# Performance work log

Measured on AMD Instinct MI355X. Metric: run time of the kernel, lower is better.

Reference implementation:

```python
import jax, jax.numpy as jnp
import numpy as np

N, E, DIN, H, DOUT = 100000, 400000, 128, 128, 128
LN_EPS = 1e-5


def _layernorm(x, g, b):
    m = jnp.mean(x, axis=-1, keepdims=True)
    v = jnp.mean((x - m) ** 2, axis=-1, keepdims=True)
    return (x - m) * jax.lax.rsqrt(v + LN_EPS) * g + b


def setup_inputs() -> dict:
    key = jax.random.key(0)
    ks = jax.random.split(key, 24)
    s = 1.0 / np.sqrt(H)
    inp = {
        'feat': jax.random.normal(ks[0], (N, DIN), jnp.float32),
        'edge_src': jax.random.randint(ks[1], (E,), 0, N, jnp.int32),
        'edge_dst': jax.random.randint(ks[2], (E,), 0, N, jnp.int32),
        'W_src': jax.random.normal(ks[3], (DIN, H), jnp.float32) * s,
        'b_src': jax.random.normal(ks[4], (H,), jnp.float32) * s,
        'W_dst': jax.random.normal(ks[5], (DIN, H), jnp.float32) * s,
        'b_dst': jax.random.normal(ks[6], (H,), jnp.float32) * s,
        'W1a': jax.random.normal(ks[7], (H, H), jnp.float32) * s,
        'W1b': jax.random.normal(ks[8], (H, H), jnp.float32) * s,
        'b1': jax.random.normal(ks[9], (H,), jnp.float32) * s,
        'W2': jax.random.normal(ks[10], (H, H), jnp.float32) * s,
        'b2': jax.random.normal(ks[11], (H,), jnp.float32) * s,
        'W3': jax.random.normal(ks[12], (H, H), jnp.float32) * s,
        'b3': jax.random.normal(ks[13], (H,), jnp.float32) * s,
        'ln_g': jnp.ones((H,), jnp.float32),
        'ln_b': jnp.zeros((H,), jnp.float32),
        'Wg1a': jax.random.normal(ks[14], (H, H), jnp.float32) * s,
        'Wg1b': jax.random.normal(ks[15], (H, H), jnp.float32) * s,
        'bg1': jax.random.normal(ks[16], (H,), jnp.float32) * s,
        'Wg2': jax.random.normal(ks[17], (H, 1), jnp.float32) * s,
        'bg2': jax.random.normal(ks[18], (1,), jnp.float32) * s,
        'W_out': jax.random.normal(ks[19], (H, DOUT), jnp.float32) * s,
        'b_out': jax.random.normal(ks[20], (DOUT,), jnp.float32) * s,
    }
    return inp


def reference(feat, edge_src, edge_dst, W_src, b_src, W_dst, b_dst,
              W1a, W1b, b1, W2, b2, W3, b3, ln_g, ln_b,
              Wg1a, Wg1b, bg1, Wg2, bg2, W_out, b_out):
    gelu = lambda x: jax.nn.gelu(x, approximate=False)  # torch nn.GELU default (erf)
    # node-level src/dst transforms, then gather per edge
    src_h = feat @ W_src + b_src                 # [N,H]
    dst_h = feat @ W_dst + b_dst                 # [N,H]
    se = src_h[edge_src]                         # [E,H]
    de = dst_h[edge_dst]                         # [E,H]
    # edge MLP on concat([se,de]) expressed as split weights (same math)
    h = gelu(se @ W1a + de @ W1b + b1)           # [E,H]
    h = gelu(h @ W2 + b2)                        # [E,H]
    msg = _layernorm(h @ W3 + b3, ln_g, ln_b)    # [E,H]
    # message gating
    gate = jax.nn.sigmoid(gelu(se @ Wg1a + de @ Wg1b + bg1) @ Wg2 + bg2)  # [E,1]
    msg = gate * msg
    # scatter-sum to destination nodes, then out transform
    upd = jax.ops.segment_sum(msg, edge_dst, num_segments=N)  # [N,H]
    return upd @ W_out + b_out                   # [N,DOUT]
```

## Files before the change

### kernel.cpp

```cpp
#include <hip/hip_runtime.h>
#include <hip/hip_bf16.h>
#include <math.h>


typedef __bf16 bf16x8 __attribute__((ext_vector_type(8)));
typedef __bf16 bf16x2 __attribute__((ext_vector_type(2)));
typedef float floatx4 __attribute__((ext_vector_type(4)));

#define LN_EPS 1e-5f

__device__ __forceinline__ unsigned short f2bf(float x) {
  unsigned int u = __float_as_uint(x);
  u = u + 0x7fffu + ((u >> 16) & 1u);
  return (unsigned short)(u >> 16);
}

__device__ __forceinline__ unsigned int pkbf(float lo, float hi) {
  bf16x2 v;
  v.x = (__bf16)lo;
  v.y = (__bf16)hi;
  return __builtin_bit_cast(unsigned int, v);
}

__device__ __forceinline__ float bf2f(unsigned short s) {
  return __uint_as_float(((unsigned int)s) << 16);
}

__device__ __forceinline__ float geluf(float x) {
  float t = x * x;
  float u = x * (2.3022080f + 0.1029434f * t);
  float e = __builtin_amdgcn_exp2f(-u);
  return x * __builtin_amdgcn_rcpf(1.0f + e);
}

__device__ __forceinline__ float sigmoidf_fast(float x) {
  float e = __builtin_amdgcn_exp2f(-1.44269504f * x);
  return __builtin_amdgcn_rcpf(1.0f + e);
}

__global__ __launch_bounds__(256) void prep_weights(
    const float* w0, const float* w1, const float* w2, const float* w3,
    const float* w4, const float* w5, const float* w6, const float* w7,
    const float* w8, unsigned short* out) {
  const float* srcs[9] = {w0, w1, w2, w3, w4, w5, w6, w7, w8};
  int m = blockIdx.x >> 2, c = blockIdx.x & 3;
  const float* src = srcs[m] + c * 32 * 128;
  __shared__ unsigned short sT[128][35];
  int tid = threadIdx.x;

  for (int it = 0; it < 4; ++it) {
    int f4 = tid + it * 256;
    float4 v = ((const float4*)src)[f4];
    int krel = f4 >> 5;
    int n0 = (f4 & 31) * 4;
    sT[n0 + 0][krel] = f2bf(v.x);
    sT[n0 + 1][krel] = f2bf(v.y);
    sT[n0 + 2][krel] = f2bf(v.z);
    sT[n0 + 3][krel] = f2bf(v.w);
  }
  __syncthreads();
  unsigned short* dst = out + m * 16384 + c * 32;
  for (int it = 0; it < 2; ++it) {
    int ch = tid + it * 256;
    int n = ch >> 2, kc = (ch & 3) * 8;
    unsigned short tmp[8];
    for (int j = 0; j < 8; ++j) tmp[j] = sT[n][kc + j];
    *(int4*)(dst + n * 128 + kc) = *(const int4*)tmp;
  }
}

#define LDB(pB, B)                                              \
  do {                                                          \
    const unsigned short* _p = (pB);                            \
    for (int kb = 0; kb < 4; ++kb) {                            \
      B[0][kb] = *(const bf16x8*)(_p + kb * 32);                \
      B[1][kb] = *(const bf16x8*)(_p + 2048 + kb * 32);         \
    }                                                           \
  } while (0)

__global__ __launch_bounds__(256, 4) void node_fused(
    const float* __restrict__ feat, const unsigned short* __restrict__ wT,
    const float* __restrict__ b_src, const float* __restrict__ b_dst,
    const float* __restrict__ b1, const float* __restrict__ bg1,
    unsigned short* __restrict__ SrcCat, unsigned short* __restrict__ DstCat,
    unsigned short* __restrict__ upd, int M) {
  __shared__ __align__(16) unsigned short sF[64][136];
  __shared__ __align__(16) unsigned short sT[64][136];
  int tid = threadIdx.x;
  int r0 = blockIdx.x * 64;

  {
    int4 z = {0, 0, 0, 0};
    int4* p = (int4*)(upd + (long long)r0 * 128);
    for (int it = 0; it < 4; ++it) {
      int idx = tid + it * 256;
      if (r0 + (idx >> 4) < M) p[idx] = z;
    }
  }

  {
    int r = tid >> 2, seg = tid & 3;
    int row = r0 + r;
    const float* src = feat + (long long)row * 128 + seg * 32;
    for (int j = 0; j < 4; ++j) {
      unsigned int tmp[4];
      if (row < M) {
        float4 f0 = *(const float4*)(src + j * 8);
        float4 f1 = *(const float4*)(src + j * 8 + 4);
        tmp[0] = pkbf(f0.x, f0.y);
        tmp[1] = pkbf(f0.z, f0.w);
        tmp[2] = pkbf(f1.x, f1.y);
        tmp[3] = pkbf(f1.z, f1.w);
      } else {
        tmp[0] = tmp[1] = tmp[2] = tmp[3] = 0;
      }
      *(int4*)&sF[r][seg * 32 + j * 8] = *(const int4*)tmp;
    }
  }
  __syncthreads();

  int w = tid >> 6, lane = tid & 63, lr = lane & 15, q = lane >> 4;
  int c0 = 32 * w + lr, c1 = c0 + 16;
  const unsigned short* pB = wT + c0 * 128 + q * 8;

  bf16x8 B[2][4];
  floatx4 accA[4][2], accP[4][2];

  auto zac = [&](floatx4 (&acc)[4][2]) {
    for (int mb = 0; mb < 4; ++mb)
      for (int nb = 0; nb < 2; ++nb) acc[mb][nb] = (floatx4){0.f, 0.f, 0.f, 0.f};
  };
  auto pass = [&](const unsigned short (*Ab)[136], floatx4 (&acc)[4][2]) {
    for (int kb = 0; kb < 4; ++kb) {
      int k = kb * 32 + q * 8;
      for (int mb = 0; mb < 4; ++mb) {
        bf16x8 a = *(const bf16x8*)&Ab[16 * mb + lr][k];
        acc[mb][0] = __builtin_amdgcn_mfma_f32_16x16x32_bf16(a, B[0][kb], acc[mb][0], 0, 0, 0);
        acc[mb][1] = __builtin_amdgcn_mfma_f32_16x16x32_bf16(a, B[1][kb], acc[mb][1], 0, 0, 0);
      }
    }
  };
  auto stage_out = [&](unsigned short (*S)[136], floatx4 (&acc)[4][2],
                       float bb0, float bb1) {
    for (int mb = 0; mb < 4; ++mb)
      for (int i = 0; i < 4; ++i) {
        int r = 16 * mb + 4 * q + i;
        unsigned int u = pkbf(acc[mb][0][i] + bb0, acc[mb][1][i] + bb1);
        S[r][c0] = (unsigned short)u;
        S[r][c1] = (unsigned short)(u >> 16);
      }
  };
  auto copy_half = [&](unsigned short* dstbase,
                       const unsigned short (*S)[136]) {
    for (int it = 0; it < 4; ++it) {
      int idx = tid + it * 256;
      int row = idx >> 4, c = idx & 15;
      if (r0 + row < M)
        *(int4*)(dstbase + (long long)(r0 + row) * 256 + c * 8) =
            *(const int4*)&S[row][c * 8];
    }
  };

  LDB(pB + 0 * 16384, B);
  zac(accA);
  pass(sF, accA);
  stage_out(sT, accA, b_src[c0], b_src[c1]);
  __syncthreads();

  LDB(pB + 2 * 16384, B);
  zac(accA);
  pass(sT, accA);
  LDB(pB + 6 * 16384, B);
  zac(accP);
  pass(sT, accP);
  __syncthreads();

  stage_out(sT, accA, b1[c0], b1[c1]);
  __syncthreads();
  copy_half(SrcCat, sT);
  __syncthreads();
  stage_out(sT, accP, bg1[c0], bg1[c1]);
  __syncthreads();
  copy_half(SrcCat + 128, sT);
  __syncthreads();

  LDB(pB + 1 * 16384, B);
  zac(accA);
  pass(sF, accA);
  stage_out(sT, accA, b_dst[c0], b_dst[c1]);
  __syncthreads();

  LDB(pB + 3 * 16384, B);
  zac(accA);
  pass(sT, accA);
  LDB(pB + 7 * 16384, B);
  zac(accP);
  pass(sT, accP);
  __syncthreads();

  stage_out(sF, accA, 0.f, 0.f);
  stage_out(sT, accP, 0.f, 0.f);
  __syncthreads();

  copy_half(DstCat, sF);
  copy_half(DstCat + 128, sT);
}

__global__ __launch_bounds__(256, 4) void gemm_out(
    const unsigned short* __restrict__ A, const unsigned short* __restrict__ Bt,
    const float* __restrict__ bias, float* __restrict__ C, int M) {
  __shared__ __align__(16) char smem[64 * 130 * 4];
  unsigned short (*sA)[136] = (unsigned short(*)[136])smem;
  float (*sO)[130] = (float(*)[130])smem;
  int tid = threadIdx.x;
  int r0 = blockIdx.x * 64;

  {
    int r = tid >> 2, seg = tid & 3;
    int row = r0 + r;
    const int4* src = (const int4*)(A + (long long)row * 128);
    for (int it = 0; it < 4; ++it) {
      int c = seg * 4 + it;
      int4 v;
      if (row < M) v = src[c];
      else v = (int4){0, 0, 0, 0};
      *(int4*)&sA[r][c * 8] = v;
    }
  }
  __syncthreads();

  int w = tid >> 6, lane = tid & 63, lr = lane & 15, q = lane >> 4;
  int c0 = 32 * w + lr, c1 = 32 * w + 16 + lr;
  const unsigned short* pB = Bt + c0 * 128 + q * 8;

  bf16x8 B[2][4];
  LDB(pB, B);
  floatx4 acc[4][2];
  for (int mb = 0; mb < 4; ++mb)
    for (int nb = 0; nb < 2; ++nb) acc[mb][nb] = (floatx4){0.f, 0.f, 0.f, 0.f};
  for (int kb = 0; kb < 4; ++kb) {
    int k = kb * 32 + q * 8;
    for (int mb = 0; mb < 4; ++mb) {
      bf16x8 a = *(const bf16x8*)&sA[16 * mb + lr][k];
      acc[mb][0] = __builtin_amdgcn_mfma_f32_16x16x32_bf16(a, B[0][kb], acc[mb][0], 0, 0, 0);
      acc[mb][1] = __builtin_amdgcn_mfma_f32_16x16x32_bf16(a, B[1][kb], acc[mb][1], 0, 0, 0);
    }
  }
  __syncthreads();

  float bv0 = bias[c0], bv1 = bias[c1];
  for (int mb = 0; mb < 4; ++mb)
    for (int i = 0; i < 4; ++i) {
      int r = 16 * mb + 4 * q + i;
      sO[r][c0] = acc[mb][0][i] + bv0;
      sO[r][c1] = acc[mb][1][i] + bv1;
    }
  __syncthreads();

  for (int it = 0; it < 8; ++it) {
    int idx = tid + it * 256;
    int row = idx >> 5, c = idx & 31;
    if (r0 + row < M)
      *(float4*)(C + (long long)(r0 + row) * 128 + c * 4) = *(const float4*)&sO[row][c * 4];
  }
}

__global__ __launch_bounds__(256, 6) void edge_fused(
    const unsigned short* __restrict__ SrcCat, const unsigned short* __restrict__ DstCat,
    const int* __restrict__ edge_src, const int* __restrict__ edge_dst,
    const unsigned short* __restrict__ wT,
    const float* __restrict__ b2, const float* __restrict__ b3,
    const float* __restrict__ ln_g, const float* __restrict__ ln_b,
    const float* __restrict__ Wg2, const float* __restrict__ bg2,
    unsigned short* __restrict__ upd, int E) {
  __shared__ __align__(16) unsigned short sH[64][136];
  __shared__ int sDst[64];
  __shared__ float sGate[64];
  __shared__ float sR1[4][64];
  __shared__ float sR2[4][64];
  __shared__ float sM[64];
  __shared__ float sRS[64];

  int tid = threadIdx.x;
  int e0 = blockIdx.x * 64;

  {
    int r = tid >> 2, seg = tid & 3;
    int e = e0 + r;
    int ee = (e < E) ? e : (E - 1);
    int es = edge_src[ee], ed = edge_dst[ee];
    if (seg == 0) sDst[r] = (e < E) ? ed : -1;
    const unsigned short* ps = SrcCat + (long long)es * 256 + seg * 32;
    const unsigned short* pd = DstCat + (long long)ed * 256 + seg * 32;

    int4 sa[4], sb[4], ga[4], gb[4];
    for (int u = 0; u < 4; ++u) {
      sa[u] = ((const int4*)ps)[u];
      sb[u] = ((const int4*)pd)[u];
      ga[u] = ((const int4*)(ps + 128))[u];
      gb[u] = ((const int4*)(pd + 128))[u];
    }
    for (int u = 0; u < 4; ++u) {
      const unsigned short* av = (const unsigned short*)&sa[u];
      const unsigned short* bv = (const unsigned short*)&sb[u];
      unsigned int ov[4];
      for (int j = 0; j < 4; ++j) {
        float g0 = geluf(bf2f(av[2 * j])     + bf2f(bv[2 * j]));
        float g1 = geluf(bf2f(av[2 * j + 1]) + bf2f(bv[2 * j + 1]));
        ov[j] = pkbf(g0, g1);
      }
      *(int4*)&sH[r][seg * 32 + u * 8] = *(const int4*)ov;
    }
    float gp = 0.f;
    for (int u = 0; u < 4; ++u) {
      const unsigned short* av = (const unsigned short*)&ga[u];
      const unsigned short* bv = (const unsigned short*)&gb[u];
      float4 w0 = *(const float4*)(Wg2 + seg * 32 + u * 8);
      float4 w1 = *(const float4*)(Wg2 + seg * 32 + u * 8 + 4);
      gp += geluf(bf2f(av[0]) + bf2f(bv[0])) * w0.x;
      gp += geluf(bf2f(av[1]) + bf2f(bv[1])) * w0.y;
      gp += geluf(bf2f(av[2]) + bf2f(bv[2])) * w0.z;
      gp += geluf(bf2f(av[3]) + bf2f(bv[3])) * w0.w;
      gp += geluf(bf2f(av[4]) + bf2f(bv[4])) * w1.x;
      gp += geluf(bf2f(av[5]) + bf2f(bv[5])) * w1.y;
      gp += geluf(bf2f(av[6]) + bf2f(bv[6])) * w1.z;
      gp += geluf(bf2f(av[7]) + bf2f(bv[7])) * w1.w;
    }
    gp += __shfl_xor(gp, 1);
    gp += __shfl_xor(gp, 2);
    if (seg == 0) sGate[r] = sigmoidf_fast(gp + bg2[0]);
  }
  __syncthreads();

  int w = tid >> 6, lane = tid & 63, lr = lane & 15, q = lane >> 4;
  int c0 = 32 * w + lr, c1 = 32 * w + 16 + lr;
  const unsigned short* pB = wT + c0 * 128 + q * 8;

  bf16x8 B[2][4];
  floatx4 acc[4][2];
  auto zacc = [&]() {
    for (int mb = 0; mb < 4; ++mb)
      for (int nb = 0; nb < 2; ++nb) acc[mb][nb] = (floatx4){0.f, 0.f, 0.f, 0.f};
  };
  auto pass = [&](const unsigned short (*Ab)[136]) {
    for (int kb = 0; kb < 4; ++kb) {
      int k = kb * 32 + q * 8;
      for (int mb = 0; mb < 4; ++mb) {
        bf16x8 a = *(const bf16x8*)&Ab[16 * mb + lr][k];
        acc[mb][0] = __builtin_amdgcn_mfma_f32_16x16x32_bf16(a, B[0][kb], acc[mb][0], 0, 0, 0);
        acc[mb][1] = __builtin_amdgcn_mfma_f32_16x16x32_bf16(a, B[1][kb], acc[mb][1], 0, 0, 0);
      }
    }
  };

  LDB(pB + 4 * 16384, B);
  zacc();
  pass(sH);
  __syncthreads();
  {
    float bv0 = b2[c0], bv1 = b2[c1];
    for (int mb = 0; mb < 4; ++mb)
      for (int i = 0; i < 4; ++i) {
        int r = 16 * mb + 4 * q + i;
        unsigned int u = pkbf(geluf(acc[mb][0][i] + bv0), geluf(acc[mb][1][i] + bv1));
        sH[r][c0] = (unsigned short)u;
        sH[r][c1] = (unsigned short)(u >> 16);
      }
  }
  __syncthreads();

  LDB(pB + 5 * 16384, B);
  zacc();
  pass(sH);
  {
    float bv0 = b3[c0], bv1 = b3[c1];
    for (int mb = 0; mb < 4; ++mb)
      for (int i = 0; i < 4; ++i) {
        float x0 = acc[mb][0][i] + bv0;
        float x1 = acc[mb][1][i] + bv1;
        acc[mb][0][i] = x0; acc[mb][1][i] = x1;
        float s = x0 + x1, s2 = x0 * x0 + x1 * x1;
        s += __shfl_xor(s, 1); s += __shfl_xor(s, 2);
        s += __shfl_xor(s, 4); s += __shfl_xor(s, 8);
        s2 += __shfl_xor(s2, 1); s2 += __shfl_xor(s2, 2);
        s2 += __shfl_xor(s2, 4); s2 += __shfl_xor(s2, 8);
        if (lr == 0) { sR1[w][16 * mb + 4 * q + i] = s; sR2[w][16 * mb + 4 * q + i] = s2; }
      }
  }
  __syncthreads();
  if (tid < 64) {
    float s = sR1[0][tid] + sR1[1][tid] + sR1[2][tid] + sR1[3][tid];
    float s2 = sR2[0][tid] + sR2[1][tid] + sR2[2][tid] + sR2[3][tid];
    float m = s * (1.f / 128.f);
    float v = s2 * (1.f / 128.f) - m * m;
    sM[tid] = m;
    sRS[tid] = rsqrtf(v + LN_EPS);
  }
  __syncthreads();

  {
    float lg0 = ln_g[c0], lg1 = ln_g[c1];
    float lb0 = ln_b[c0], lb1 = ln_b[c1];
    for (int mb = 0; mb < 4; ++mb)
      for (int i = 0; i < 4; ++i) {
        int r = 16 * mb + 4 * q + i;
        int dst = sDst[r];
        float m = sM[r], rs = sRS[r], gt = sGate[r];
        float v0 = ((acc[mb][0][i] - m) * rs * lg0 + lb0) * gt;
        float v1 = ((acc[mb][1][i] - m) * rs * lg1 + lb1) * gt;
        float o0 = __shfl_xor(v0, 1);
        float o1 = __shfl_xor(v1, 1);
        if (dst >= 0) {
          unsigned int pk;
          int colb;
          if ((lr & 1) == 0) {
            pk = pkbf(v0, o0);
            colb = c0;
          } else {
            pk = pkbf(o1, v1);
            colb = c0 + 15;
          }
          unsigned short* addr = upd + (long long)dst * 128 + colb;
          asm volatile("global_atomic_pk_add_bf16 %0, %1, off"
                       :: "v"(addr), "v"(pk) : "memory");
        }
      }
  }
}

extern "C" void kernel_launch(void* const* d_in, const int* in_sizes, int n_in,
                              void* d_out, int out_size, void* d_ws, size_t ws_size,
                              hipStream_t stream) {
  const float* feat   = (const float*)d_in[0];
  const int* edge_src = (const int*)d_in[1];
  const int* edge_dst = (const int*)d_in[2];
  const float* W_src = (const float*)d_in[3];  const float* b_src = (const float*)d_in[4];
  const float* W_dst = (const float*)d_in[5];  const float* b_dst = (const float*)d_in[6];
  const float* W1a = (const float*)d_in[7];    const float* W1b = (const float*)d_in[8];
  const float* b1  = (const float*)d_in[9];
  const float* W2  = (const float*)d_in[10];   const float* b2  = (const float*)d_in[11];
  const float* W3  = (const float*)d_in[12];   const float* b3  = (const float*)d_in[13];
  const float* ln_g = (const float*)d_in[14];  const float* ln_b = (const float*)d_in[15];
  const float* Wg1a = (const float*)d_in[16];  const float* Wg1b = (const float*)d_in[17];
  const float* bg1  = (const float*)d_in[18];
  const float* Wg2  = (const float*)d_in[19];  const float* bg2 = (const float*)d_in[20];
  const float* W_out = (const float*)d_in[21]; const float* b_out = (const float*)d_in[22];

  int N = in_sizes[0] / 128;
  int E = in_sizes[1];

  char* ws = (char*)d_ws;
  unsigned short* wT = (unsigned short*)ws;
  size_t off = 9 * 16384 * sizeof(unsigned short);
  unsigned short* SrcCat = (unsigned short*)(ws + off);
  off += (size_t)N * 256 * sizeof(unsigned short);
  unsigned short* DstCat = (unsigned short*)(ws + off);
  off += (size_t)N * 256 * sizeof(unsigned short);
  unsigned short* upd = (unsigned short*)(ws + off);

  prep_weights<<<36, 256, 0, stream>>>(W_src, W_dst, W1a, W1b, W2, W3, Wg1a, Wg1b,
                                       W_out, wT);
  int mtiles = (N + 63) / 64;
  node_fused<<<mtiles, 256, 0, stream>>>(feat, wT, b_src, b_dst, b1, bg1,
                                         SrcCat, DstCat, upd, N);
  edge_fused<<<(E + 63) / 64, 256, 0, stream>>>(SrcCat, DstCat, edge_src, edge_dst,
                                                wT, b2, b3, ln_g, ln_b, Wg2, bg2,
                                                upd, E);
  gemm_out<<<mtiles, 256, 0, stream>>>(upd, wT + 8 * 16384, b_out, (float*)d_out, N);
}
```

Baseline: 393.3 us.

## Restructure node_fused so each wave owns 16 rows, removing block barriers

```diff
diff --git a/kernel.cpp b/kernel.cpp
--- a/kernel.cpp
+++ b/kernel.cpp
@@ -6,6 +6,7 @@
 typedef __bf16 bf16x8 __attribute__((ext_vector_type(8)));
 typedef __bf16 bf16x2 __attribute__((ext_vector_type(2)));
 typedef float floatx4 __attribute__((ext_vector_type(4)));
+typedef unsigned int uintx4 __attribute__((ext_vector_type(4)));
 
 #define LN_EPS 1e-5f
 
@@ -20,6 +21,11 @@
   v.x = (__bf16)lo;
   v.y = (__bf16)hi;
   return __builtin_bit_cast(unsigned int, v);
+}
+
+__device__ __forceinline__ unsigned short f2bfh(float x) {
+  __bf16 h = (__bf16)x;
+  return __builtin_bit_cast(unsigned short, h);
 }
 
 __device__ __forceinline__ float bf2f(unsigned short s) {
@@ -84,76 +90,86 @@
     const float* __restrict__ b1, const float* __restrict__ bg1,
     unsigned short* __restrict__ SrcCat, unsigned short* __restrict__ DstCat,
     unsigned short* __restrict__ upd, int M) {
-  __shared__ __align__(16) unsigned short sF[64][136];
-  __shared__ __align__(16) unsigned short sT[64][136];
+  __shared__ __align__(16) unsigned short sW[4][16][136];
+  __shared__ __align__(16) unsigned short sU[4][16][136];
   int tid = threadIdx.x;
-  int r0 = blockIdx.x * 64;
+  int w = tid >> 6, lane = tid & 63, lr = lane & 15, q = lane >> 4;
+  int r0 = blockIdx.x * 64 + w * 16;
+
+  unsigned short (*mW)[136] = sW[w];
+  unsigned short (*mU)[136] = sU[w];
 
   {
     int4 z = {0, 0, 0, 0};
-    int4* p = (int4*)(upd + (long long)r0 * 128);
-    for (int it = 0; it < 4; ++it) {
-      int idx = tid + it * 256;
-      if (r0 + (idx >> 4) < M) p[idx] = z;
-    }
-  }
-
-  {
-    int r = tid >> 2, seg = tid & 3;
-    int row = r0 + r;
-    const float* src = feat + (long long)row * 128 + seg * 32;
+#pragma unroll
     for (int j = 0; j < 4; ++j) {
-      unsigned int tmp[4];
-      if (row < M) {
-        float4 f0 = *(const float4*)(src + j * 8);
-        float4 f1 = *(const float4*)(src + j * 8 + 4);
-        tmp[0] = pkbf(f0.x, f0.y);
-        tmp[1] = pkbf(f0.z, f0.w);
-        tmp[2] = pkbf(f1.x, f1.y);
-        tmp[3] = pkbf(f1.z, f1.w);
-      } else {
-        tmp[0] = tmp[1] = tmp[2] = tmp[3] = 0;
-      }
-      *(int4*)&sF[r][seg * 32 + j * 8] = *(const int4*)tmp;
-    }
-  }
-  __syncthreads();
-
-  int w = tid >> 6, lane = tid & 63, lr = lane & 15, q = lane >> 4;
-  int c0 = 32 * w + lr, c1 = c0 + 16;
-  const unsigned short* pB = wT + c0 * 128 + q * 8;
-
-  bf16x8 B[2][4];
-  floatx4 accA[4][2], accP[4][2];
-
-  auto zac = [&](floatx4 (&acc)[4][2]) {
-    for (int mb = 0; mb < 4; ++mb)
-      for (int nb = 0; nb < 2; ++nb) acc[mb][nb] = (floatx4){0.f, 0.f, 0.f, 0.f};
-  };
-  auto pass = [&](const unsigned short (*Ab)[136], floatx4 (&acc)[4][2]) {
+      int idx = lane + j * 64;
+      int row = idx >> 4, c = idx & 15;
+      if (r0 + row < M)
+        ((int4*)(upd + (long long)(r0 + row) * 128))[c] = z;
+    }
+  }
+
+  bf16x8 fA[4];
+  {
+    int frow = r0 + lr;
+    bool fok = frow < M;
+    const float* fp = feat + (long long)frow * 128 + q * 8;
+#pragma unroll
     for (int kb = 0; kb < 4; ++kb) {
-      int k = kb * 32 + q * 8;
-      for (int mb = 0; mb < 4; ++mb) {
-        bf16x8 a = *(const bf16x8*)&Ab[16 * mb + lr][k];
-        acc[mb][0] = __builtin_amdgcn_mfma_f32_16x16x32_bf16(a, B[0][kb], acc[mb][0], 0, 0, 0);
-        acc[mb][1] = __builtin_amdgcn_mfma_f32_16x16x32_bf16(a, B[1][kb], acc[mb][1], 0, 0, 0);
-      }
-    }
-  };
-  auto stage_out = [&](unsigned short (*S)[136], floatx4 (&acc)[4][2],
-                       float bb0, float bb1) {
-    for (int mb = 0; mb < 4; ++mb)
-      for (int i = 0; i < 4; ++i) {
-        int r = 16 * mb + 4 * q + i;
-        unsigned int u = pkbf(acc[mb][0][i] + bb0, acc[mb][1][i] + bb1);
-        S[r][c0] = (unsigned short)u;
-        S[r][c1] = (unsigned short)(u >> 16);
-      }
-  };
-  auto copy_half = [&](unsigned short* dstbase,
-                       const unsigned short (*S)[136]) {
-    for (int it = 0; it < 4; ++it) {
-      int idx = tid + it * 256;
+      float4 a = {0.f, 0.f, 0.f, 0.f}, b = {0.f, 0.f, 0.f, 0.f};
+      if (fok) {
+        a = *(const float4*)(fp + kb * 32);
+        b = *(const float4*)(fp + kb * 32 + 4);
+      }
+      uintx4 u;
+      u.x = pkbf(a.x, a.y);
+      u.y = pkbf(a.z, a.w);
+      u.z = pkbf(b.x, b.y);
+      u.w = pkbf(b.z, b.w);
+      fA[kb] = __builtin_bit_cast(bf16x8, u);
+    }
+  }
+
+  floatx4 acc[8];
+  bf16x8 hA[4];
+
+  auto zacc = [&]() {
+#pragma unroll
+    for (int nt = 0; nt < 8; ++nt) acc[nt] = (floatx4){0.f, 0.f, 0.f, 0.f};
+  };
+  auto gemm = [&](const unsigned short* wbase, const bf16x8 (&Af)[4]) {
+#pragma unroll
+    for (int nt = 0; nt < 8; ++nt) {
+      const unsigned short* bp = wbase + (nt * 16 + lr) * 128 + q * 8;
+      bf16x8 B0 = *(const bf16x8*)(bp);
+      bf16x8 B1 = *(const bf16x8*)(bp + 32);
+      bf16x8 B2 = *(const bf16x8*)(bp + 64);
+      bf16x8 B3 = *(const bf16x8*)(bp + 96);
+      acc[nt] = __builtin_amdgcn_mfma_f32_16x16x32_bf16(Af[0], B0, acc[nt], 0, 0, 0);
+      acc[nt] = __builtin_amdgcn_mfma_f32_16x16x32_bf16(Af[1], B1, acc[nt], 0, 0, 0);
+      acc[nt] = __builtin_amdgcn_mfma_f32_16x16x32_bf16(Af[2], B2, acc[nt], 0, 0, 0);
+      acc[nt] = __builtin_amdgcn_mfma_f32_16x16x32_bf16(Af[3], B3, acc[nt], 0, 0, 0);
+    }
+  };
+  auto stage = [&](unsigned short (*S)[136], const float* bias) {
+#pragma unroll
+    for (int nt = 0; nt < 8; ++nt) {
+      float bv = bias ? bias[nt * 16 + lr] : 0.f;
+#pragma unroll
+      for (int i = 0; i < 4; ++i)
+        S[4 * q + i][nt * 16 + lr] = f2bfh(acc[nt][i] + bv);
+    }
+  };
+  auto loadA = [&](unsigned short (*S)[136]) {
+#pragma unroll
+    for (int kb = 0; kb < 4; ++kb)
+      hA[kb] = *(const bf16x8*)&S[lr][kb * 32 + q * 8];
+  };
+  auto copy16 = [&](unsigned short* dstbase, const unsigned short (*S)[136]) {
+#pragma unroll
+    for (int j = 0; j < 4; ++j) {
+      int idx = lane + j * 64;
       int row = idx >> 4, c = idx & 15;
       if (r0 + row < M)
         *(int4*)(dstbase + (long long)(r0 + row) * 256 + c * 8) =
@@ -161,49 +177,31 @@
     }
   };
 
-  LDB(pB + 0 * 16384, B);
-  zac(accA);
-  pass(sF, accA);
-  stage_out(sT, accA, b_src[c0], b_src[c1]);
-  __syncthreads();
-
-  LDB(pB + 2 * 16384, B);
-  zac(accA);
-  pass(sT, accA);
-  LDB(pB + 6 * 16384, B);
-  zac(accP);
-  pass(sT, accP);
-  __syncthreads();
-
-  stage_out(sT, accA, b1[c0], b1[c1]);
-  __syncthreads();
-  copy_half(SrcCat, sT);
-  __syncthreads();
-  stage_out(sT, accP, bg1[c0], bg1[c1]);
-  __syncthreads();
-  copy_half(SrcCat + 128, sT);
-  __syncthreads();
-
-  LDB(pB + 1 * 16384, B);
-  zac(accA);
-  pass(sF, accA);
-  stage_out(sT, accA, b_dst[c0], b_dst[c1]);
-  __syncthreads();
-
-  LDB(pB + 3 * 16384, B);
-  zac(accA);
-  pass(sT, accA);
-  LDB(pB + 7 * 16384, B);
-  zac(accP);
-  pass(sT, accP);
-  __syncthreads();
-
-  stage_out(sF, accA, 0.f, 0.f);
-  stage_out(sT, accP, 0.f, 0.f);
-  __syncthreads();
-
-  copy_half(DstCat, sF);
-  copy_half(DstCat + 128, sT);
+  zacc();
+  gemm(wT + 0 * 16384, fA);
+  stage(mW, b_src);
+  loadA(mW);
+  zacc();
+  gemm(wT + 2 * 16384, hA);
+  stage(mU, b1);
+  copy16(SrcCat, mU);
+  zacc();
+  gemm(wT + 6 * 16384, hA);
+  stage(mU, bg1);
+  copy16(SrcCat + 128, mU);
+
+  zacc();
+  gemm(wT + 1 * 16384, fA);
+  stage(mW, b_dst);
+  loadA(mW);
+  zacc();
+  gemm(wT + 3 * 16384, hA);
+  stage(mU, nullptr);
+  copy16(DstCat, mU);
+  zacc();
+  gemm(wT + 7 * 16384, hA);
+  stage(mU, nullptr);
+  copy16(DstCat + 128, mU);
 }
 
 __global__ __launch_bounds__(256, 4) void gemm_out(
```

Measured after the change: 463.7 us. +17.9%, slower.
